# Kernel optimization log

Measured on AMD Instinct MI355X. Metric: run time of the kernel, lower is better.

Reference implementation:

```python
import jax, jax.numpy as jnp
import numpy as np

B, T, C, H = 4, 4096, 1024, 64

def setup_inputs() -> dict:
    key = jax.random.key(0)
    kx, kq, kk, kv = jax.random.split(key, 4)
    x = jax.random.normal(kx, (B, T, C), dtype=jnp.float32)
    Wq = jax.random.normal(kq, (C, H), dtype=jnp.float32) * (C ** -0.5)
    Wk = jax.random.normal(kk, (C, H), dtype=jnp.float32) * (C ** -0.5)
    Wv = jax.random.normal(kv, (C, H), dtype=jnp.float32) * (C ** -0.5)
    return {"x": x, "Wq": Wq, "Wk": Wk, "Wv": Wv}

def reference(x, Wq, Wk, Wv):
    # single-head causal attention, dropout p=0 (eval)
    q = jnp.einsum('btc,ch->bth', x, Wq)  # [B,T,H]
    k = jnp.einsum('btc,ch->bth', x, Wk)
    v = jnp.einsum('btc,ch->bth', x, Wv)
    scale = k.shape[-1] ** -0.5
    scores = jnp.einsum('bth,bsh->bts', q, k) * scale  # [B,T,T]
    causal = jnp.tril(jnp.ones((q.shape[1], q.shape[1]), dtype=bool))
    scores = jnp.where(causal, scores, -jnp.inf)
    weights = jax.nn.softmax(scores, axis=-1)
    out = jnp.einsum('bts,bsh->bth', weights, v)  # [B,T,H]
    return out
```

## Files before the change

### kernel.cpp

```cpp
#include <hip/hip_runtime.h>


typedef short  s16x8 __attribute__((ext_vector_type(8)));
typedef float  f32x4 __attribute__((ext_vector_type(4)));
typedef unsigned u32x2 __attribute__((ext_vector_type(2)));

constexpr int B = 4, T = 4096, C = 1024, H = 64;
constexpr int M = B * T;
constexpr float LOG2E = 1.44269504088896340736f;
constexpr float QSCALE = 0.125f * LOG2E;
constexpr float MBASE  = 4.0f * LOG2E;

__device__ __forceinline__ unsigned short f2bf(float f) {
    union { float f; unsigned u; } v; v.f = f;
    unsigned r = v.u + 0x7fffu + ((v.u >> 16) & 1u);
    return (unsigned short)(r >> 16);
}

__device__ __forceinline__ unsigned cvt_pk_bf16(float lo, float hi) {
    unsigned r;
    asm("v_cvt_pk_bf16_f32 %0, %1, %2" : "=v"(r) : "v"(lo), "v"(hi));
    return r;
}

__device__ __forceinline__ void gl_lds16(const void* g, void* l) {
    __builtin_amdgcn_global_load_lds(
        (const __attribute__((address_space(1))) unsigned*)g,
        (__attribute__((address_space(3))) unsigned*)l, 16, 0, 0);
}

__global__ void prep_w(const float* __restrict__ Wq, const float* __restrict__ Wk,
                       const float* __restrict__ Wv, unsigned short* __restrict__ Wt) {
    const int n = blockIdx.x;
    const float* W = (n < 64) ? Wq : (n < 128 ? Wk : Wv);
    const int col = n & 63;
    for (int k = threadIdx.x; k < C; k += blockDim.x)
        Wt[(size_t)n * C + k] = f2bf(W[(size_t)k * H + col]);
}

__global__ __launch_bounds__(512) void qkv_proj(
    const float* __restrict__ x, const unsigned short* __restrict__ Wt,
    unsigned short* __restrict__ Q, unsigned short* __restrict__ K,
    unsigned short* __restrict__ V) {
    __shared__ __align__(16) unsigned short ldsA[2][32 * 64];
    __shared__ __align__(16) unsigned short ldsB[2][192 * 64];

    const int t = threadIdx.x, lane = t & 63, w = t >> 6;
    const int i = lane & 15, g = lane >> 4;
    const int rowbase = blockIdx.x * 32;
    const int rw = w & 1, nw = w >> 1;

    const int arow = t >> 3, aslot = t & 7;
    const float* aga = x + (size_t)(rowbase + arow) * C + ((aslot ^ (arow & 7)) * 8);
    const int awoff = arow * 64 + aslot * 8;
    const bool astage = (t < 256);

    const int brow8 = lane >> 3, bslot = lane & 7;
    const unsigned short* bga[3];
    int bn0[3];
#pragma unroll
    for (int j = 0; j < 3; ++j) {
        bn0[j] = w * 24 + j * 8;
        bga[j] = Wt + (size_t)(bn0[j] + brow8) * C + ((bslot ^ brow8) * 8);
    }

    f32x4 acc[3];
#pragma unroll
    for (int n = 0; n < 3; ++n) acc[n] = (f32x4){0.f, 0.f, 0.f, 0.f};

    {
#pragma unroll
        for (int j = 0; j < 3; ++j)
            gl_lds16(bga[j], &ldsB[0][bn0[j] * 64]);
        if (astage) {
            f32x4 a0 = *(const f32x4*)(aga);
            f32x4 a1 = *(const f32x4*)(aga + 4);
            union { unsigned u[4]; s16x8 v; } av;
            av.u[0] = cvt_pk_bf16(a0[0], a0[1]);
            av.u[1] = cvt_pk_bf16(a0[2], a0[3]);
            av.u[2] = cvt_pk_bf16(a1[0], a1[1]);
            av.u[3] = cvt_pk_bf16(a1[2], a1[3]);
            *(s16x8*)&ldsA[0][awoff] = av.v;
        }
    }
    __syncthreads();

    for (int it = 0; it < 16; ++it) {
        const int cur = it & 1, nxt = cur ^ 1;
        const int kc = (it + 1) * 64;
        f32x4 a0, a1;
        const bool more = (it < 15);
        if (more) {
            if (astage) {
                a0 = *(const f32x4*)(aga + kc);
                a1 = *(const f32x4*)(aga + kc + 4);
            }
#pragma unroll
            for (int j = 0; j < 3; ++j)
                gl_lds16(bga[j] + kc, &ldsB[nxt][bn0[j] * 64]);
        }
#pragma unroll
        for (int kst = 0; kst < 2; ++kst) {
            const int c = kst * 4 + g;
            s16x8 a = *(const s16x8*)&ldsA[cur][(rw * 16 + i) * 64 + ((c ^ (i & 7)) * 8)];
#pragma unroll
            for (int nt = 0; nt < 3; ++nt) {
                int n = nw * 48 + nt * 16 + i;
                s16x8 b = *(const s16x8*)&ldsB[cur][n * 64 + ((c ^ (i & 7)) * 8)];
                acc[nt] = __builtin_amdgcn_mfma_f32_16x16x32_bf16(a, b, acc[nt], 0, 0, 0);
            }
        }
        if (more && astage) {
            union { unsigned u[4]; s16x8 v; } av;
            av.u[0] = cvt_pk_bf16(a0[0], a0[1]);
            av.u[1] = cvt_pk_bf16(a0[2], a0[3]);
            av.u[2] = cvt_pk_bf16(a1[0], a1[1]);
            av.u[3] = cvt_pk_bf16(a1[2], a1[3]);
            *(s16x8*)&ldsA[nxt][awoff] = av.v;
        }
        __syncthreads();
    }

#pragma unroll
    for (int nt = 0; nt < 3; ++nt) {
        int n = nw * 48 + nt * 16 + i;
#pragma unroll
        for (int r = 0; r < 4; ++r) {
            int row = rowbase + rw * 16 + g * 4 + r;
            float val = acc[nt][r];
            if (n < 64)       Q[(size_t)row * H + n]         = f2bf(val * QSCALE);
            else if (n < 128) K[(size_t)row * H + (n - 64)]  = f2bf(val);
            else              V[(size_t)row * H + (n - 128)] = f2bf(val);
        }
    }
}

__global__ __launch_bounds__(256) void vtrans(const unsigned short* __restrict__ V,
                                              unsigned short* __restrict__ VT) {
    __shared__ __align__(16) unsigned short tile[64][72];
    const int b = blockIdx.x >> 6, t0 = (blockIdx.x & 63) * 64;
    const int tid = threadIdx.x;
    {
        int row = tid >> 2, col = (tid & 3) * 16;
        s16x8 v0 = *(const s16x8*)(V + (size_t)(b * T + t0 + row) * H + col);
        s16x8 v1 = *(const s16x8*)(V + (size_t)(b * T + t0 + row) * H + col + 8);
        *(s16x8*)&tile[row][col]     = v0;
        *(s16x8*)&tile[row][col + 8] = v1;
    }
    __syncthreads();
    {
        int h = tid >> 2, tcol = (tid & 3) * 16;
        s16x8 o0, o1;
#pragma unroll
        for (int j = 0; j < 8; ++j) {
            int pos = tcol + j, c = pos >> 5, pp = pos & 31;
            int tok = (c << 5) | (((pp >> 2) & 1) << 4) | ((pp >> 3) << 2) | (pp & 3);
            o0[j] = (short)tile[tok][h];
        }
#pragma unroll
        for (int j = 0; j < 8; ++j) {
            int pos = tcol + 8 + j, c = pos >> 5, pp = pos & 31;
            int tok = (c << 5) | (((pp >> 2) & 1) << 4) | ((pp >> 3) << 2) | (pp & 3);
            o1[j] = (short)tile[tok][h];
        }
        unsigned short* dst = VT + (size_t)(b * H + h) * T + t0 + tcol;
        *(s16x8*)dst       = o0;
        *(s16x8*)(dst + 8) = o1;
    }
}

__global__ __launch_bounds__(512, 4) void attn(
    const unsigned short* __restrict__ Qg, const unsigned short* __restrict__ Kg,
    const unsigned short* __restrict__ VTg,
    unsigned short* __restrict__ Opb, float* __restrict__ lpart) {
    __shared__ __align__(16) unsigned short ks[2][64 * 64];
    __shared__ __align__(16) unsigned short vs[2][64 * 64];

    const int t = threadIdx.x, lane = t & 63, w = t >> 6;
    const int bid = blockIdx.x;
    const int b = bid & 3;
    const int sp = (bid >> 2) & 7;
    const int qt = 31 - (bid >> 5);
    const int q0 = qt * 128;
    const int q0w = q0 + w * 16;
    const int i = lane & 15, g = lane >> 4, g4 = g * 4;
    const int nkv = 2 * qt + 2;

    const unsigned short* Kb = Kg  + (size_t)b * T * H;
    const unsigned short* Vb = VTg + (size_t)b * H * T;

    const int srow = t >> 3, sl = t & 7, sx = sl ^ (srow & 7);
    const unsigned short* kga = Kb + (size_t)srow * H + sx * 8;
    const unsigned short* vga = Vb + (size_t)srow * T + sx * 8;
    const int soff = srow * 64 + sl * 8;

    const unsigned short* Qrow = Qg + (size_t)(b * T + q0w + i) * H;
    s16x8 bq0 = *(const s16x8*)(Qrow + g * 8);
    s16x8 bq1 = *(const s16x8*)(Qrow + 32 + g * 8);

    f32x4 oacc[4];
#pragma unroll
    for (int nt = 0; nt < 4; ++nt) oacc[nt] = (f32x4){0.f, 0.f, 0.f, 0.f};
    float l_run = 0.f;

    if (sp < nkv) {
        const size_t kv0 = (size_t)sp * 64;
        gl_lds16(kga + kv0 * H, &ks[0][soff]);
        gl_lds16(vga + kv0,     &vs[0][soff]);
    }
    __syncthreads();

    int cur = 0;
    for (int tile = sp; tile < nkv; tile += 8) {
        const int kv = tile * 64;
        if (tile + 8 < nkv) {
            const size_t kvn = (size_t)kv + 512;
            gl_lds16(kga + kvn * H, &ks[cur ^ 1][soff]);
            gl_lds16(vga + kvn,     &vs[cur ^ 1][soff]);
        }

        if (kv <= q0w + 15) {
            s16x8 kb[8], vb[8];
#pragma unroll
            for (int kst = 0; kst < 2; ++kst)
#pragma unroll
                for (int nt = 0; nt < 4; ++nt) {
                    const int off = (nt * 16 + i) * 64 + (((kst * 4 + g) ^ (i & 7)) * 8);
                    kb[kst * 4 + nt] = *(const s16x8*)&ks[cur][off];
                    vb[kst * 4 + nt] = *(const s16x8*)&vs[cur][off];
                }

            f32x4 s[4];
#pragma unroll
            for (int nt = 0; nt < 4; ++nt)
                s[nt] = (f32x4){-MBASE, -MBASE, -MBASE, -MBASE};
#pragma unroll
            for (int nt = 0; nt < 4; ++nt)
                s[nt] = __builtin_amdgcn_mfma_f32_16x16x32_bf16(kb[nt], bq0, s[nt], 0, 0, 0);
#pragma unroll
            for (int nt = 0; nt < 4; ++nt)
                s[nt] = __builtin_amdgcn_mfma_f32_16x16x32_bf16(kb[4 + nt], bq1, s[nt], 0, 0, 0);

            if (kv + 63 > q0w) {
                const int thr = q0w + i - kv;
#pragma unroll
                for (int nt = 0; nt < 4; ++nt)
#pragma unroll
                    for (int r = 0; r < 4; ++r)
                        if (nt * 16 + g4 + r > thr) s[nt][r] = -INFINITY;
            }

#pragma unroll
            for (int nt = 0; nt < 4; ++nt)
#pragma unroll
                for (int r = 0; r < 4; ++r)
                    s[nt][r] = exp2f(s[nt][r]);

#pragma unroll
            for (int kst = 0; kst < 2; ++kst) {
                union { unsigned u[4]; s16x8 v; } pb;
                pb.u[0] = cvt_pk_bf16(s[2 * kst][0],     s[2 * kst][1]);
                pb.u[1] = cvt_pk_bf16(s[2 * kst][2],     s[2 * kst][3]);
                pb.u[2] = cvt_pk_bf16(s[2 * kst + 1][0], s[2 * kst + 1][1]);
                pb.u[3] = cvt_pk_bf16(s[2 * kst + 1][2], s[2 * kst + 1][3]);
#pragma unroll
                for (int nt = 0; nt < 4; ++nt)
                    oacc[nt] = __builtin_amdgcn_mfma_f32_16x16x32_bf16(vb[kst * 4 + nt], pb.v, oacc[nt], 0, 0, 0);
            }

            l_run += ((s[0][0] + s[0][1]) + (s[0][2] + s[0][3]))
                   + ((s[1][0] + s[1][1]) + (s[1][2] + s[1][3]))
                   + ((s[2][0] + s[2][1]) + (s[2][2] + s[2][3]))
                   + ((s[3][0] + s[3][1]) + (s[3][2] + s[3][3]));
        }

        __syncthreads();
        cur ^= 1;
    }

    l_run += __shfl_xor(l_run, 16);
    l_run += __shfl_xor(l_run, 32);
    unsigned short* op = Opb + ((size_t)bid * 128 + w * 16 + i) * 64;
#pragma unroll
    for (int nt = 0; nt < 4; ++nt) {
        u32x2 pk;
        pk[0] = cvt_pk_bf16(oacc[nt][0], oacc[nt][1]);
        pk[1] = cvt_pk_bf16(oacc[nt][2], oacc[nt][3]);
        *(u32x2*)(op + nt * 16 + g4) = pk;
    }
    if (g == 0) lpart[(size_t)bid * 128 + w * 16 + i] = l_run;
}

__global__ __launch_bounds__(256) void merge8(
    const unsigned short* __restrict__ Opb, const float* __restrict__ lpart,
    float* __restrict__ out) {
    const int idx = blockIdx.x * 256 + threadIdx.x;
    const int row = idx >> 4, c4 = (idx & 15) * 4;
    const int b = row >> 12, q = row & 4095;
    const int qt = q >> 7, r = q & 127;
    const int qti = 31 - qt;

    float L = 0.f;
    f32x4 o = (f32x4){0.f, 0.f, 0.f, 0.f};
#pragma unroll
    for (int sp = 0; sp < 8; ++sp) {
        const int bidp = qti * 32 + sp * 4 + b;
        L += lpart[(size_t)bidp * 128 + r];
        union { unsigned long long d; unsigned short s[4]; } v;
        v.d = *(const unsigned long long*)&Opb[((size_t)bidp * 128 + r) * 64 + c4];
#pragma unroll
        for (int k = 0; k < 4; ++k) {
            union { unsigned u; float f; } cv;
            cv.u = (unsigned)v.s[k] << 16;
            o[k] += cv.f;
        }
    }
    const float inv = 1.0f / L;
    f32x4 res = (f32x4){o[0] * inv, o[1] * inv, o[2] * inv, o[3] * inv};
    *(f32x4*)&out[(size_t)row * 64 + c4] = res;
}

extern "C" void kernel_launch(void* const* d_in, const int* in_sizes, int n_in,
                              void* d_out, int out_size, void* d_ws, size_t ws_size,
                              hipStream_t stream) {
    (void)in_sizes; (void)n_in; (void)out_size; (void)ws_size;
    const float* x  = (const float*)d_in[0];
    const float* Wq = (const float*)d_in[1];
    const float* Wk = (const float*)d_in[2];
    const float* Wv = (const float*)d_in[3];
    float* out = (float*)d_out;

    char* ws = (char*)d_ws;
    unsigned short* Q  = (unsigned short*)(ws);
    unsigned short* K  = (unsigned short*)(ws + (size_t)1 * M * H * 2);
    unsigned short* V  = (unsigned short*)(ws + (size_t)2 * M * H * 2);
    unsigned short* VT = (unsigned short*)(ws + (size_t)3 * M * H * 2);
    unsigned short* Wt = (unsigned short*)(ws + (size_t)4 * M * H * 2);
    unsigned short* Opb = (unsigned short*)(ws + (size_t)4 * M * H * 2 + 512 * 1024);
    float* lpart = (float*)(ws + (size_t)4 * M * H * 2 + 512 * 1024
                            + (size_t)1024 * 128 * 64 * 2);

    prep_w<<<192, 256, 0, stream>>>(Wq, Wk, Wv, Wt);
    qkv_proj<<<M / 32, 512, 0, stream>>>(x, Wt, Q, K, V);
    vtrans<<<B * (T / 64), 256, 0, stream>>>(V, VT);
    attn<<<1024, 512, 0, stream>>>(Q, K, VT, Opb, lpart);
    merge8<<<1024, 256, 0, stream>>>(Opb, lpart, out);
}
```

Before: 55.56 us.

## Fuse V transpose into projection epilogue and give each attention wave 32 query rows

The QKV projection now writes V directly in the permuted transposed layout the attention kernel expects, so the separate vtrans kernel and its extra global round trip go away. The attention kernel drops to 256 threads, and each wave handles two 16-row query groups. Each K/V tile loaded from LDS is reused across twice as many query rows, and the cooperative staging loop issues two loads per thread. This cuts LDS reads and the launch count, but raises register pressure from doubled accumulators and halves the waves per block.

```diff
diff --git a/kernel.cpp b/kernel.cpp
--- a/kernel.cpp
+++ b/kernel.cpp
@@ -41,7 +41,7 @@
 __global__ __launch_bounds__(512) void qkv_proj(
     const float* __restrict__ x, const unsigned short* __restrict__ Wt,
     unsigned short* __restrict__ Q, unsigned short* __restrict__ K,
-    unsigned short* __restrict__ V) {
+    unsigned short* __restrict__ VT) {
     __shared__ __align__(16) unsigned short ldsA[2][32 * 64];
     __shared__ __align__(16) unsigned short ldsB[2][192 * 64];
 
@@ -123,53 +123,28 @@
 
 #pragma unroll
     for (int nt = 0; nt < 3; ++nt) {
-        int n = nw * 48 + nt * 16 + i;
-#pragma unroll
-        for (int r = 0; r < 4; ++r) {
-            int row = rowbase + rw * 16 + g * 4 + r;
-            float val = acc[nt][r];
-            if (n < 64)       Q[(size_t)row * H + n]         = f2bf(val * QSCALE);
-            else if (n < 128) K[(size_t)row * H + (n - 64)]  = f2bf(val);
-            else              V[(size_t)row * H + (n - 128)] = f2bf(val);
-        }
-    }
-}
-
-__global__ __launch_bounds__(256) void vtrans(const unsigned short* __restrict__ V,
-                                              unsigned short* __restrict__ VT) {
-    __shared__ __align__(16) unsigned short tile[64][72];
-    const int b = blockIdx.x >> 6, t0 = (blockIdx.x & 63) * 64;
-    const int tid = threadIdx.x;
-    {
-        int row = tid >> 2, col = (tid & 3) * 16;
-        s16x8 v0 = *(const s16x8*)(V + (size_t)(b * T + t0 + row) * H + col);
-        s16x8 v1 = *(const s16x8*)(V + (size_t)(b * T + t0 + row) * H + col + 8);
-        *(s16x8*)&tile[row][col]     = v0;
-        *(s16x8*)&tile[row][col + 8] = v1;
-    }
-    __syncthreads();
-    {
-        int h = tid >> 2, tcol = (tid & 3) * 16;
-        s16x8 o0, o1;
-#pragma unroll
-        for (int j = 0; j < 8; ++j) {
-            int pos = tcol + j, c = pos >> 5, pp = pos & 31;
-            int tok = (c << 5) | (((pp >> 2) & 1) << 4) | ((pp >> 3) << 2) | (pp & 3);
-            o0[j] = (short)tile[tok][h];
-        }
-#pragma unroll
-        for (int j = 0; j < 8; ++j) {
-            int pos = tcol + 8 + j, c = pos >> 5, pp = pos & 31;
-            int tok = (c << 5) | (((pp >> 2) & 1) << 4) | ((pp >> 3) << 2) | (pp & 3);
-            o1[j] = (short)tile[tok][h];
-        }
-        unsigned short* dst = VT + (size_t)(b * H + h) * T + t0 + tcol;
-        *(s16x8*)dst       = o0;
-        *(s16x8*)(dst + 8) = o1;
-    }
-}
-
-__global__ __launch_bounds__(512, 4) void attn(
+        const int base = nw * 48 + nt * 16;
+        const int n = base + i;
+        if (base >= 128) {
+            const int h = n - 128;
+            const int bb = rowbase >> 12, tb = rowbase & 4095;
+            u32x2 pk;
+            pk[0] = cvt_pk_bf16(acc[nt][0], acc[nt][1]);
+            pk[1] = cvt_pk_bf16(acc[nt][2], acc[nt][3]);
+            *(u32x2*)(VT + (size_t)(bb * H + h) * T + tb + g * 8 + rw * 4) = pk;
+        } else if (base >= 64) {
+#pragma unroll
+            for (int r = 0; r < 4; ++r)
+                K[(size_t)(rowbase + rw * 16 + g * 4 + r) * H + (n - 64)] = f2bf(acc[nt][r]);
+        } else {
+#pragma unroll
+            for (int r = 0; r < 4; ++r)
+                Q[(size_t)(rowbase + rw * 16 + g * 4 + r) * H + n] = f2bf(acc[nt][r] * QSCALE);
+        }
+    }
+}
+
+__global__ __launch_bounds__(256) void attn(
     const unsigned short* __restrict__ Qg, const unsigned short* __restrict__ Kg,
     const unsigned short* __restrict__ VTg,
     unsigned short* __restrict__ Opb, float* __restrict__ lpart) {
@@ -182,31 +157,38 @@
     const int sp = (bid >> 2) & 7;
     const int qt = 31 - (bid >> 5);
     const int q0 = qt * 128;
-    const int q0w = q0 + w * 16;
+    const int q0w = q0 + w * 32;
     const int i = lane & 15, g = lane >> 4, g4 = g * 4;
     const int nkv = 2 * qt + 2;
 
     const unsigned short* Kb = Kg  + (size_t)b * T * H;
     const unsigned short* Vb = VTg + (size_t)b * H * T;
 
-    const int srow = t >> 3, sl = t & 7, sx = sl ^ (srow & 7);
-    const unsigned short* kga = Kb + (size_t)srow * H + sx * 8;
-    const unsigned short* vga = Vb + (size_t)srow * T + sx * 8;
-    const int soff = srow * 64 + sl * 8;
-
-    const unsigned short* Qrow = Qg + (size_t)(b * T + q0w + i) * H;
-    s16x8 bq0 = *(const s16x8*)(Qrow + g * 8);
-    s16x8 bq1 = *(const s16x8*)(Qrow + 32 + g * 8);
-
-    f32x4 oacc[4];
-#pragma unroll
-    for (int nt = 0; nt < 4; ++nt) oacc[nt] = (f32x4){0.f, 0.f, 0.f, 0.f};
-    float l_run = 0.f;
+    const int r8 = lane >> 3, sl = lane & 7, sx = sl ^ r8;
+
+    const unsigned short* QrowA = Qg + (size_t)(b * T + q0w + i) * H;
+    s16x8 bqa0 = *(const s16x8*)(QrowA + g * 8);
+    s16x8 bqa1 = *(const s16x8*)(QrowA + 32 + g * 8);
+    const unsigned short* QrowB = QrowA + 16 * H;
+    s16x8 bqb0 = *(const s16x8*)(QrowB + g * 8);
+    s16x8 bqb1 = *(const s16x8*)(QrowB + 32 + g * 8);
+
+    f32x4 oa[4], ob[4];
+#pragma unroll
+    for (int nt = 0; nt < 4; ++nt) {
+        oa[nt] = (f32x4){0.f, 0.f, 0.f, 0.f};
+        ob[nt] = (f32x4){0.f, 0.f, 0.f, 0.f};
+    }
+    float la = 0.f, lb = 0.f;
 
     if (sp < nkv) {
-        const size_t kv0 = (size_t)sp * 64;
-        gl_lds16(kga + kv0 * H, &ks[0][soff]);
-        gl_lds16(vga + kv0,     &vs[0][soff]);
+        const int kv0 = sp * 64;
+#pragma unroll
+        for (int j = 0; j < 2; ++j) {
+            const int row = (w + j * 4) * 8 + r8;
+            gl_lds16(Kb + (size_t)(kv0 + row) * H + sx * 8, &ks[0][row * 64 + sl * 8]);
+            gl_lds16(Vb + (size_t)row * T + kv0 + sx * 8,   &vs[0][row * 64 + sl * 8]);
+        }
     }
     __syncthreads();
 
@@ -214,81 +196,141 @@
     for (int tile = sp; tile < nkv; tile += 8) {
         const int kv = tile * 64;
         if (tile + 8 < nkv) {
-            const size_t kvn = (size_t)kv + 512;
-            gl_lds16(kga + kvn * H, &ks[cur ^ 1][soff]);
-            gl_lds16(vga + kvn,     &vs[cur ^ 1][soff]);
-        }
-
-        if (kv <= q0w + 15) {
-            s16x8 kb[8], vb[8];
+            const int kvn = kv + 512;
+#pragma unroll
+            for (int j = 0; j < 2; ++j) {
+                const int row = (w + j * 4) * 8 + r8;
+                gl_lds16(Kb + (size_t)(kvn + row) * H + sx * 8, &ks[cur ^ 1][row * 64 + sl * 8]);
+                gl_lds16(Vb + (size_t)row * T + kvn + sx * 8,   &vs[cur ^ 1][row * 64 + sl * 8]);
+            }
+        }
+
+        if (kv <= q0w + 31) {
+            s16x8 kb[8];
 #pragma unroll
             for (int kst = 0; kst < 2; ++kst)
 #pragma unroll
+                for (int nt = 0; nt < 4; ++nt)
+                    kb[kst * 4 + nt] = *(const s16x8*)
+                        &ks[cur][(nt * 16 + i) * 64 + (((kst * 4 + g) ^ (i & 7)) * 8)];
+
+            unsigned pa[8], pb2[8];
+
+            {
+                f32x4 s[4];
+#pragma unroll
+                for (int nt = 0; nt < 4; ++nt)
+                    s[nt] = (f32x4){-MBASE, -MBASE, -MBASE, -MBASE};
+#pragma unroll
+                for (int nt = 0; nt < 4; ++nt)
+                    s[nt] = __builtin_amdgcn_mfma_f32_16x16x32_bf16(kb[nt], bqa0, s[nt], 0, 0, 0);
+#pragma unroll
+                for (int nt = 0; nt < 4; ++nt)
+                    s[nt] = __builtin_amdgcn_mfma_f32_16x16x32_bf16(kb[4 + nt], bqa1, s[nt], 0, 0, 0);
+                if (kv + 63 > q0w) {
+                    const int thr = q0w + i - kv;
+#pragma unroll
+                    for (int nt = 0; nt < 4; ++nt)
+#pragma unroll
+                        for (int r = 0; r < 4; ++r)
+                            if (nt * 16 + g4 + r > thr) s[nt][r] = -INFINITY;
+                }
+#pragma unroll
+                for (int nt = 0; nt < 4; ++nt)
+#pragma unroll
+                    for (int r = 0; r < 4; ++r)
+                        s[nt][r] = exp2f(s[nt][r]);
+#pragma unroll
                 for (int nt = 0; nt < 4; ++nt) {
-                    const int off = (nt * 16 + i) * 64 + (((kst * 4 + g) ^ (i & 7)) * 8);
-                    kb[kst * 4 + nt] = *(const s16x8*)&ks[cur][off];
-                    vb[kst * 4 + nt] = *(const s16x8*)&vs[cur][off];
-                }
-
-            f32x4 s[4];
-#pragma unroll
-            for (int nt = 0; nt < 4; ++nt)
-                s[nt] = (f32x4){-MBASE, -MBASE, -MBASE, -MBASE};
-#pragma unroll
-            for (int nt = 0; nt < 4; ++nt)
-                s[nt] = __builtin_amdgcn_mfma_f32_16x16x32_bf16(kb[nt], bq0, s[nt], 0, 0, 0);
-#pragma unroll
-            for (int nt = 0; nt < 4; ++nt)
-                s[nt] = __builtin_amdgcn_mfma_f32_16x16x32_bf16(kb[4 + nt], bq1, s[nt], 0, 0, 0);
-
-            if (kv + 63 > q0w) {
-                const int thr = q0w + i - kv;
+                    pa[nt * 2]     = cvt_pk_bf16(s[nt][0], s[nt][1]);
+                    pa[nt * 2 + 1] = cvt_pk_bf16(s[nt][2], s[nt][3]);
+                }
+                la += ((s[0][0] + s[0][1]) + (s[0][2] + s[0][3]))
+                    + ((s[1][0] + s[1][1]) + (s[1][2] + s[1][3]))
+                    + ((s[2][0] + s[2][1]) + (s[2][2] + s[2][3]))
+                    + ((s[3][0] + s[3][1]) + (s[3][2] + s[3][3]));
+            }
+
+            {
+                f32x4 s[4];
+#pragma unroll
+                for (int nt = 0; nt < 4; ++nt)
+                    s[nt] = (f32x4){-MBASE, -MBASE, -MBASE, -MBASE};
+#pragma unroll
+                for (int nt = 0; nt < 4; ++nt)
+                    s[nt] = __builtin_amdgcn_mfma_f32_16x16x32_bf16(kb[nt], bqb0, s[nt], 0, 0, 0);
+#pragma unroll
+                for (int nt = 0; nt < 4; ++nt)
+                    s[nt] = __builtin_amdgcn_mfma_f32_16x16x32_bf16(kb[4 + nt], bqb1, s[nt], 0, 0, 0);
+                if (kv + 63 > q0w + 16) {
+                    const int thr = q0w + 16 + i - kv;
+#pragma unroll
+                    for (int nt = 0; nt < 4; ++nt)
+#pragma unroll
+                        for (int r = 0; r < 4; ++r)
+                            if (nt * 16 + g4 + r > thr) s[nt][r] = -INFINITY;
+                }
 #pragma unroll
                 for (int nt = 0; nt < 4; ++nt)
 #pragma unroll
                     for (int r = 0; r < 4; ++r)
-                        if (nt * 16 + g4 + r > thr) s[nt][r] = -INFINITY;
-            }
-
-#pragma unroll
-            for (int nt = 0; nt < 4; ++nt)
-#pragma unroll
-                for (int r = 0; r < 4; ++r)
-                    s[nt][r] = exp2f(s[nt][r]);
+                        s[nt][r] = exp2f(s[nt][r]);
+#pragma unroll
+                for (int nt = 0; nt < 4; ++nt) {
+                    pb2[nt * 2]     = cvt_pk_bf16(s[nt][0], s[nt][1]);
+                    pb2[nt * 2 + 1] = cvt_pk_bf16(s[nt][2], s[nt][3]);
+                }
+                lb += ((s[0][0] + s[0][1]) + (s[0][2] + s[0][3]))
+                    + ((s[1][0] + s[1][1]) + (s[1][2] + s[1][3]))
+                    + ((s[2][0] + s[2][1]) + (s[2][2] + s[2][3]))
+                    + ((s[3][0] + s[3][1]) + (s[3][2] + s[3][3]));
+            }
+
+            s16x8 vb[8];
+#pragma unroll
+            for (int kst = 0; kst < 2; ++kst)
+#pragma unroll
+                for (int nt = 0; nt < 4; ++nt)
+                    vb[kst * 4 + nt] = *(const s16x8*)
+                        &vs[cur][(nt * 16 + i) * 64 + (((kst * 4 + g) ^ (i & 7)) * 8)];
 
 #pragma unroll
             for (int kst = 0; kst < 2; ++kst) {
-                union { unsigned u[4]; s16x8 v; } pb;
-                pb.u[0] = cvt_pk_bf16(s[2 * kst][0],     s[2 * kst][1]);
-                pb.u[1] = cvt_pk_bf16(s[2 * kst][2],     s[2 * kst][3]);
-                pb.u[2] = cvt_pk_bf16(s[2 * kst + 1][0], s[2 * kst + 1][1]);
-                pb.u[3] = cvt_pk_bf16(s[2 * kst + 1][2], s[2 * kst + 1][3]);
-#pragma unroll
-                for (int nt = 0; nt < 4; ++nt)
-                    oacc[nt] = __builtin_amdgcn_mfma_f32_16x16x32_bf16(vb[kst * 4 + nt], pb.v, oacc[nt], 0, 0, 0);
-            }
-
-            l_run += ((s[0][0] + s[0][1]) + (s[0][2] + s[0][3]))
-                   + ((s[1][0] + s[1][1]) + (s[1][2] + s[1][3]))
-                   + ((s[2][0] + s[2][1]) + (s[2][2] + s[2][3]))
-                   + ((s[3][0] + s[3][1]) + (s[3][2] + s[3][3]));
+                union { unsigned u[4]; s16x8 v; } fa, fb;
+                fa.u[0] = pa[4 * kst];      fa.u[1] = pa[4 * kst + 1];
+                fa.u[2] = pa[4 * kst + 2];  fa.u[3] = pa[4 * kst + 3];
+                fb.u[0] = pb2[4 * kst];     fb.u[1] = pb2[4 * kst + 1];
+                fb.u[2] = pb2[4 * kst + 2]; fb.u[3] = pb2[4 * kst + 3];
+#pragma unroll
+                for (int nt = 0; nt < 4; ++nt) {
+                    oa[nt] = __builtin_amdgcn_mfma_f32_16x16x32_bf16(vb[kst * 4 + nt], fa.v, oa[nt], 0, 0, 0);
+                    ob[nt] = __builtin_amdgcn_mfma_f32_16x16x32_bf16(vb[kst * 4 + nt], fb.v, ob[nt], 0, 0, 0);
+                }
+            }
         }
 
         __syncthreads();
         cur ^= 1;
     }
 
-    l_run += __shfl_xor(l_run, 16);
-    l_run += __shfl_xor(l_run, 32);
-    unsigned short* op = Opb + ((size_t)bid * 128 + w * 16 + i) * 64;
+    la += __shfl_xor(la, 16);  la += __shfl_xor(la, 32);
+    lb += __shfl_xor(lb, 16);  lb += __shfl_xor(lb, 32);
+    unsigned short* opA = Opb + ((size_t)bid * 128 + w * 32 + i) * 64;
+    unsigned short* opB = opA + 16 * 64;
 #pragma unroll
     for (int nt = 0; nt < 4; ++nt) {
         u32x2 pk;
-        pk[0] = cvt_pk_bf16(oacc[nt][0], oacc[nt][1]);
-        pk[1] = cvt_pk_bf16(oacc[nt][2], oacc[nt][3]);
-        *(u32x2*)(op + nt * 16 + g4) = pk;
-    }
-    if (g == 0) lpart[(size_t)bid * 128 + w * 16 + i] = l_run;
+        pk[0] = cvt_pk_bf16(oa[nt][0], oa[nt][1]);
+        pk[1] = cvt_pk_bf16(oa[nt][2], oa[nt][3]);
+        *(u32x2*)(opA + nt * 16 + g4) = pk;
+        pk[0] = cvt_pk_bf16(ob[nt][0], ob[nt][1]);
+        pk[1] = cvt_pk_bf16(ob[nt][2], ob[nt][3]);
+        *(u32x2*)(opB + nt * 16 + g4) = pk;
+    }
+    if (g == 0) {
+        lpart[(size_t)bid * 128 + w * 32 + i]      = la;
+        lpart[(size_t)bid * 128 + w * 32 + 16 + i] = lb;
+    }
 }
 
 __global__ __launch_bounds__(256) void merge8(
@@ -333,7 +375,6 @@
     char* ws = (char*)d_ws;
     unsigned short* Q  = (unsigned short*)(ws);
     unsigned short* K  = (unsigned short*)(ws + (size_t)1 * M * H * 2);
-    unsigned short* V  = (unsigned short*)(ws + (size_t)2 * M * H * 2);
     unsigned short* VT = (unsigned short*)(ws + (size_t)3 * M * H * 2);
     unsigned short* Wt = (unsigned short*)(ws + (size_t)4 * M * H * 2);
     unsigned short* Opb = (unsigned short*)(ws + (size_t)4 * M * H * 2 + 512 * 1024);
@@ -341,8 +382,7 @@
                             + (size_t)1024 * 128 * 64 * 2);
 
     prep_w<<<192, 256, 0, stream>>>(Wq, Wk, Wv, Wt);
-    qkv_proj<<<M / 32, 512, 0, stream>>>(x, Wt, Q, K, V);
-    vtrans<<<B * (T / 64), 256, 0, stream>>>(V, VT);
-    attn<<<1024, 512, 0, stream>>>(Q, K, VT, Opb, lpart);
+    qkv_proj<<<M / 32, 512, 0, stream>>>(x, Wt, Q, K, VT);
+    attn<<<1024, 256, 0, stream>>>(Q, K, VT, Opb, lpart);
     merge8<<<1024, 256, 0, stream>>>(Opb, lpart, out);
 }
```

After: 56.03 us. No clear change (+0.8%).
